# Performance work log

Hardware: AMD Instinct MI355X
Metric: run time of the kernel (lower is better)

Reference implementation:

```python
import jax, jax.numpy as jnp
import numpy as np

N = 10000      # nodes
E = 320000     # edges (avg degree 32)
D_IN = 128
D_H = 256
D_C = 32       # comm_dim
D_OUT = 64


def setup_inputs() -> dict:
    key = jax.random.key(0)
    ks = jax.random.split(key, 14)
    p = lambda k, shape: jax.random.normal(k, shape, jnp.float32) * 0.02
    return {
        "x": jax.random.normal(ks[0], (N, D_IN), jnp.float32),
        "edge_index": jax.random.randint(ks[1], (2, E), 0, N),
        "W_in": p(ks[2], (D_IN, D_H)), "b_in": jnp.zeros((D_H,), jnp.float32),
        "Wq": p(ks[3], (D_H, D_C)),   "bq": jnp.zeros((D_C,), jnp.float32),
        "Wk": p(ks[4], (D_H, D_C)),   "bk": jnp.zeros((D_C,), jnp.float32),
        "Wv": p(ks[5], (D_H, D_H)),   "bv": jnp.zeros((D_H,), jnp.float32),
        "W1": p(ks[6], (2 * D_H, D_H)), "b1": jnp.zeros((D_H,), jnp.float32),
        "W2": p(ks[7], (D_H, D_OUT)),  "b2": jnp.zeros((D_OUT,), jnp.float32),
    }


def reference(x, edge_index, W_in, b_in, Wq, bq, Wk, bk, Wv, bv, W1, b1, W2, b2):
    n = x.shape[0]
    h = x @ W_in + b_in                       # [N, D_H]
    q = h @ Wq + bq                           # [N, D_C]
    k = h @ Wk + bk                           # [N, D_C]
    v = h @ Wv + bv                           # [N, D_H]
    scores = (q @ k.T) / np.sqrt(q.shape[-1]).astype(np.float32)  # [N, N]
    # torch: zeros -> scatter 1 at edges -> masked_fill(==0, -inf);
    # edge positions keep value 1.0 ADDED to scores (faithful quirk).
    mask = jnp.full((n, n), -jnp.inf, jnp.float32)
    mask = mask.at[edge_index[0], edge_index[1]].set(1.0)
    w = jax.nn.softmax(scores + mask, axis=-1)
    w = jnp.nan_to_num(w, nan=0.0)            # rows with no edges -> all zeros
    comm = w @ v                              # [N, D_H]
    combined = jnp.concatenate([h, comm], axis=-1)  # [N, 2*D_H]
    return jax.nn.relu(combined @ W1 + b1) @ W2 + b2  # [N, D_OUT]
```

## Files before the change

### kernel.cpp

```cpp
#include <hip/hip_runtime.h>
#include <stdint.h>
#include <stddef.h>

constexpr int N_NODES = 10000;
constexpr int N_EDGES = 320000;
constexpr int DIM_IN  = 128;
constexpr int DIM_H   = 256;
constexpr int DIM_C   = 32;
constexpr int DIM_OUT = 64;
constexpr int DIM_QKV = DIM_C + DIM_C + DIM_H;
constexpr int DIM_QK  = 2 * DIM_C;
constexpr int DIM_CAT = 2 * DIM_H;
constexpr float SCALE = 0.17677669529663687f;
constexpr int MAXD = 192;
constexpr float VSCALE = 64.0f;
constexpr int PAD = 40;
constexpr int HP  = 264;

#if __has_builtin(__builtin_amdgcn_cvt_pk_f32_fp8) && __has_builtin(__builtin_amdgcn_cvt_pk_fp8_f32)
#define V_FP8 1
#else
#define V_FP8 0
#endif

constexpr size_t alignw(size_t w) { return (w + 15) & ~size_t(15); }
constexpr size_t OFF_DEG   = 0;
constexpr size_t OFF_COL   = alignw(OFF_DEG + N_NODES);
constexpr size_t OFF_QK    = alignw(OFF_COL + (size_t)N_NODES * MAXD);
constexpr size_t OFF_BQKV  = alignw(OFF_QK + (size_t)N_NODES * DIM_QK);
constexpr size_t OFF_VT    = alignw(OFF_BQKV + DIM_QKV);
constexpr size_t OFF_CATBF = alignw(OFF_VT + (size_t)N_NODES * DIM_H / 2);
constexpr size_t OFF_WINT  = alignw(OFF_CATBF + (size_t)N_NODES * DIM_CAT / 2);
constexpr size_t OFF_WQKVT = alignw(OFF_WINT + (size_t)DIM_H * DIM_IN / 2);
constexpr size_t OFF_W1T   = alignw(OFF_WQKVT + (size_t)DIM_QKV * DIM_H / 2);
constexpr size_t OFF_W2T   = alignw(OFF_W1T + (size_t)DIM_H * DIM_CAT / 2);

typedef __attribute__((ext_vector_type(8))) short short8;
typedef __attribute__((ext_vector_type(4))) float floatx4;
typedef __attribute__((ext_vector_type(2))) float floatx2;

#define MFMA16 __builtin_amdgcn_mfma_f32_16x16x32_bf16

__device__ inline unsigned short f2bf(float f) {
    uint32_t u = __builtin_bit_cast(uint32_t, f);
    uint32_t r = (u + 0x7fffu + ((u >> 16) & 1u)) >> 16;
    return (unsigned short)r;
}
__device__ inline float bf2f_lo(uint32_t u) { return __builtin_bit_cast(float, u << 16); }
__device__ inline float bf2f_hi(uint32_t u) { return __builtin_bit_cast(float, u & 0xffff0000u); }

__global__ void prep(const int* __restrict__ ei,
                     const float* __restrict__ W_in,
                     const float* __restrict__ Wq, const float* __restrict__ Wk,
                     const float* __restrict__ Wv,
                     const float* __restrict__ bq, const float* __restrict__ bk,
                     const float* __restrict__ bv,
                     const float* __restrict__ W1, const float* __restrict__ W2,
                     int* __restrict__ deg, int* __restrict__ col,
                     unsigned short* __restrict__ WinT, unsigned short* __restrict__ WqkvT,
                     unsigned short* __restrict__ W1T, unsigned short* __restrict__ W2T,
                     float* __restrict__ bqkv)
{
    const int i0 = blockIdx.x * blockDim.x + threadIdx.x;
    const int stride = gridDim.x * blockDim.x;
    for (int e = i0; e < N_EDGES; e += stride) {
        int src = ei[e];
        int dst = ei[N_EDGES + e];
        int slot = atomicAdd(&deg[src], 1);
        if (slot < MAXD) col[src * MAXD + slot] = dst;
    }
    for (int idx = i0; idx < DIM_IN * DIM_H; idx += stride) {
        int k = idx >> 8, n = idx & 255;
        WinT[n * DIM_IN + k] = f2bf(W_in[idx]);
    }
    for (int idx = i0; idx < DIM_H * DIM_C; idx += stride) {
        int k = idx >> 5, n = idx & 31;
        WqkvT[n * DIM_H + k] = f2bf(Wq[idx]);
    }
    for (int idx = i0; idx < DIM_H * DIM_C; idx += stride) {
        int k = idx >> 5, n = idx & 31;
        WqkvT[(DIM_C + n) * DIM_H + k] = f2bf(Wk[idx]);
    }
    for (int idx = i0; idx < DIM_H * DIM_H; idx += stride) {
        int k = idx >> 8, n = idx & 255;
        WqkvT[(2 * DIM_C + n) * DIM_H + k] = f2bf(Wv[idx]);
    }
    for (int idx = i0; idx < DIM_CAT * DIM_H; idx += stride) {
        int k = idx >> 8, n = idx & 255;
        W1T[n * DIM_CAT + k] = f2bf(W1[idx]);
    }
    for (int idx = i0; idx < DIM_H * DIM_OUT; idx += stride) {
        int k = idx >> 6, n = idx & 63;
        W2T[n * DIM_H + k] = f2bf(W2[idx]);
    }
    for (int idx = i0; idx < DIM_QKV; idx += stride)
        bqkv[idx] = (idx < DIM_C) ? bq[idx]
                  : (idx < 2 * DIM_C) ? bk[idx - DIM_C] : bv[idx - 2 * DIM_C];
}

__global__ __launch_bounds__(256)
void gemm12(const float* __restrict__ x,
            const unsigned short* __restrict__ WinT, const float* __restrict__ b_in,
            const unsigned short* __restrict__ WqkvT, const float* __restrict__ bqkv,
            unsigned short* __restrict__ cat_bf, float* __restrict__ qk,
            unsigned short* __restrict__ v_tab)
{
    __shared__ short hS[32 * HP];
    __shared__ short As[32 * PAD];
    __shared__ short Bs[320 * PAD];
    const int tid   = threadIdx.x;
    const int wave  = tid >> 6;
    const int lane  = tid & 63;
    const int quad  = lane >> 4;
    const int col16 = lane & 15;
    const int sr    = tid >> 2;
    const int sc    = (tid & 3) * 8;
    const int ar    = tid >> 3;
    const int ac    = (tid & 7) * 4;
    const int row0  = blockIdx.x * 32;

    floatx4 acc[2][4] = {};
    for (int k0 = 0; k0 < DIM_IN; k0 += 32) {
        {
            int gr = row0 + ar;
            float4 a = {};
            if (gr < N_NODES) a = *(const float4*)(x + (size_t)gr * DIM_IN + k0 + ac);
            uint2 o;
            o.x = (uint32_t)f2bf(a.x) | ((uint32_t)f2bf(a.y) << 16);
            o.y = (uint32_t)f2bf(a.z) | ((uint32_t)f2bf(a.w) << 16);
            *(uint2*)(As + ar * PAD + ac) = o;
        }
        #pragma unroll
        for (int p = 0; p < 4; ++p) {
            int r = sr + p * 64;
            *(short8*)(Bs + r * PAD + sc) = *(const short8*)(WinT + (size_t)r * DIM_IN + k0 + sc);
        }
        __syncthreads();
        short8 af[2], bfr[4];
        #pragma unroll
        for (int m = 0; m < 2; ++m)
            af[m] = *(const short8*)(As + (m * 16 + col16) * PAD + quad * 8);
        #pragma unroll
        for (int n = 0; n < 4; ++n)
            bfr[n] = *(const short8*)(Bs + (wave * 64 + n * 16 + col16) * PAD + quad * 8);
        #pragma unroll
        for (int m = 0; m < 2; ++m)
            #pragma unroll
            for (int n = 0; n < 4; ++n)
                acc[m][n] = MFMA16(af[m], bfr[n], acc[m][n], 0, 0, 0);
        __syncthreads();
    }
    #pragma unroll
    for (int m = 0; m < 2; ++m)
        #pragma unroll
        for (int n = 0; n < 4; ++n) {
            int gc = wave * 64 + n * 16 + col16;
            float bia = b_in[gc];
            #pragma unroll
            for (int r = 0; r < 4; ++r) {
                int lr = m * 16 + quad * 4 + r;
                unsigned short hv = f2bf(acc[m][n][r] + bia);
                hS[lr * HP + gc] = (short)hv;
                if (row0 + lr < N_NODES) cat_bf[(size_t)(row0 + lr) * DIM_CAT + gc] = hv;
            }
        }
    __syncthreads();

    floatx4 acc2[2][5] = {};
    for (int k0 = 0; k0 < DIM_H; k0 += 32) {
        #pragma unroll
        for (int p = 0; p < 5; ++p) {
            int r = sr + p * 64;
            *(short8*)(Bs + r * PAD + sc) = *(const short8*)(WqkvT + (size_t)r * DIM_H + k0 + sc);
        }
        __syncthreads();
        short8 af[2], bfr[5];
        #pragma unroll
        for (int m = 0; m < 2; ++m)
            af[m] = *(const short8*)(hS + (m * 16 + col16) * HP + k0 + quad * 8);
        #pragma unroll
        for (int n = 0; n < 5; ++n)
            bfr[n] = *(const short8*)(Bs + (wave * 80 + n * 16 + col16) * PAD + quad * 8);
        #pragma unroll
        for (int m = 0; m < 2; ++m)
            #pragma unroll
            for (int n = 0; n < 5; ++n)
                acc2[m][n] = MFMA16(af[m], bfr[n], acc2[m][n], 0, 0, 0);
        __syncthreads();
    }
    #pragma unroll
    for (int m = 0; m < 2; ++m)
        #pragma unroll
        for (int n = 0; n < 5; ++n) {
            int gc = wave * 80 + n * 16 + col16;
            float bia = bqkv[gc];
            #pragma unroll
            for (int r = 0; r < 4; ++r) {
                int gr = row0 + m * 16 + quad * 4 + r;
                if (gr >= N_NODES) continue;
                float v = acc2[m][n][r] + bia;
                if (gc < DIM_QK) {
                    qk[(size_t)gr * DIM_QK + gc] = v;
                } else {
#if V_FP8
                    int pk = __builtin_amdgcn_cvt_pk_fp8_f32(v * VSCALE, 0.f, 0, false);
                    ((unsigned char*)v_tab)[(size_t)gr * DIM_H + (gc - DIM_QK)] =
                        (unsigned char)(pk & 0xff);
#else
                    v_tab[(size_t)gr * DIM_H + (gc - DIM_QK)] = f2bf(v);
#endif
                }
            }
        }
}

__global__ __launch_bounds__(256)
void attn_row(const float* __restrict__ qk, const unsigned short* __restrict__ v_tab,
              const int* __restrict__ deg, const int* __restrict__ col,
              unsigned short* __restrict__ cat_bf) {
    __shared__ int   dstS[4][MAXD];
    __shared__ float wS[4][MAXD];
    __shared__ float qS[4][DIM_C];
    const int wave = threadIdx.x >> 6;
    const int lane = threadIdx.x & 63;
    const int row = blockIdx.x * 4 + wave;
    int d = deg[row];
    if (d > MAXD) d = MAXD;
    const int* crow = col + (size_t)row * MAXD;

    for (int p = lane; p < d; p += 64) dstS[wave][p] = crow[p];
    if (lane < DIM_C) qS[wave][lane] = qk[(size_t)row * DIM_QK + lane];
    __syncthreads();

    float mysum = 0.f;
    if (d <= 64) {
        int mydst = (lane < d) ? dstS[wave][lane] : -1;
        bool dup = false;
        for (int k2 = 0; k2 < d - 1; ++k2) {
            int other = __shfl(mydst, k2, 64);
            dup = dup || (k2 < lane && other == mydst);
        }
        float w = 0.f;
        if (lane < d && !dup) {
            const float4* kp = (const float4*)(qk + (size_t)mydst * DIM_QK + DIM_C);
            float s = 0.f;
            #pragma unroll
            for (int i = 0; i < DIM_C / 4; ++i) {
                float4 b = kp[i];
                s += qS[wave][4 * i + 0] * b.x + qS[wave][4 * i + 1] * b.y
                   + qS[wave][4 * i + 2] * b.z + qS[wave][4 * i + 3] * b.w;
            }
            w = expf(s * SCALE);
        }
        wS[wave][lane] = w;
        mysum = w;
    } else {
        for (int p = lane; p < d; p += 64) {
            int mydst = dstS[wave][p];
            bool dup = false;
            for (int j = 0; j < p; ++j) dup = dup || (dstS[wave][j] == mydst);
            float w = 0.f;
            if (!dup) {
                const float4* kp = (const float4*)(qk + (size_t)mydst * DIM_QK + DIM_C);
                float s = 0.f;
                #pragma unroll
                for (int i = 0; i < DIM_C / 4; ++i) {
                    float4 b = kp[i];
                    s += qS[wave][4 * i + 0] * b.x + qS[wave][4 * i + 1] * b.y
                       + qS[wave][4 * i + 2] * b.z + qS[wave][4 * i + 3] * b.w;
                }
                w = expf(s * SCALE);
            }
            wS[wave][p] = w;
            mysum += w;
        }
    }
    #pragma unroll
    for (int off = 32; off; off >>= 1) mysum += __shfl_down(mysum, off, 64);
    float total = __shfl(mysum, 0, 64);
#if V_FP8
    float inv = (d > 0 && total > 0.f) ? 1.0f / (total * VSCALE) : 0.f;
#else
    float inv = (d > 0 && total > 0.f) ? 1.0f / total : 0.f;
#endif
    __syncthreads();

    float4 acc = make_float4(0.f, 0.f, 0.f, 0.f);
#if V_FP8
    const uint32_t* vb = (const uint32_t*)v_tab;
#else
    const uint2* vb = (const uint2*)v_tab;
#endif
    for (int p0 = 0; p0 < d; p0 += 16) {
        int j[16]; float w[16];
        #pragma unroll
        for (int t = 0; t < 16; ++t) {
            int idx = p0 + t;
            bool in = idx < d;
            j[t] = in ? dstS[wave][idx] : 0;
            w[t] = in ? wS[wave][idx] : 0.f;
        }
#if V_FP8
        uint32_t r[16];
        #pragma unroll
        for (int t = 0; t < 16; ++t) r[t] = vb[(size_t)j[t] * 64 + lane];
        #pragma unroll
        for (int t = 0; t < 16; ++t) {
            floatx2 lo = __builtin_amdgcn_cvt_pk_f32_fp8(r[t], false);
            floatx2 hi = __builtin_amdgcn_cvt_pk_f32_fp8(r[t], true);
            acc.x += w[t] * lo.x; acc.y += w[t] * lo.y;
            acc.z += w[t] * hi.x; acc.w += w[t] * hi.y;
        }
#else
        uint2 r[16];
        #pragma unroll
        for (int t = 0; t < 16; ++t) r[t] = vb[(size_t)j[t] * 64 + lane];
        #pragma unroll
        for (int t = 0; t < 16; ++t) {
            acc.x += w[t] * bf2f_lo(r[t].x);
            acc.y += w[t] * bf2f_hi(r[t].x);
            acc.z += w[t] * bf2f_lo(r[t].y);
            acc.w += w[t] * bf2f_hi(r[t].y);
        }
#endif
    }
    acc.x *= inv; acc.y *= inv; acc.z *= inv; acc.w *= inv;
    uint2 o;
    o.x = (uint32_t)f2bf(acc.x) | ((uint32_t)f2bf(acc.y) << 16);
    o.y = (uint32_t)f2bf(acc.z) | ((uint32_t)f2bf(acc.w) << 16);
    *(uint2*)(cat_bf + (size_t)row * DIM_CAT + DIM_H + lane * 4) = o;
}

__global__ __launch_bounds__(256)
void gemm_w1w2(const unsigned short* __restrict__ cat, const unsigned short* __restrict__ W1T,
               const float* __restrict__ b1, const unsigned short* __restrict__ W2T,
               const float* __restrict__ b2, float* __restrict__ out, int M)
{
    constexpr int TP = 260;
    __shared__ short As[32 * PAD];
    __shared__ short BsTs[256 * PAD];
    short* Bs = BsTs;
    short* Ts = BsTs;
    const int tid   = threadIdx.x;
    const int wave  = tid >> 6;
    const int lane  = tid & 63;
    const int quad  = lane >> 4;
    const int col16 = lane & 15;
    const int row0  = blockIdx.x * 32;

    const int sr = tid >> 2;
    const int sc = (tid & 3) * 8;

    floatx4 acc[2][4] = {};
    for (int k0 = 0; k0 < DIM_CAT; k0 += 32) {
        if (sr < 32) {
            int gr = row0 + sr;
            short8 v = {};
            if (gr < M) v = *(const short8*)(cat + (size_t)gr * DIM_CAT + k0 + sc);
            *(short8*)(As + sr * PAD + sc) = v;
        }
        #pragma unroll
        for (int p = 0; p < 4; ++p) {
            int r = sr + p * 64;
            *(short8*)(Bs + r * PAD + sc) = *(const short8*)(W1T + (size_t)r * DIM_CAT + k0 + sc);
        }
        __syncthreads();
        short8 af[2], bfr[4];
        #pragma unroll
        for (int m = 0; m < 2; ++m)
            af[m] = *(const short8*)(As + (m * 16 + col16) * PAD + quad * 8);
        #pragma unroll
        for (int n = 0; n < 4; ++n)
            bfr[n] = *(const short8*)(Bs + (wave * 64 + n * 16 + col16) * PAD + quad * 8);
        #pragma unroll
        for (int m = 0; m < 2; ++m)
            #pragma unroll
            for (int n = 0; n < 4; ++n)
                acc[m][n] = MFMA16(af[m], bfr[n], acc[m][n], 0, 0, 0);
        __syncthreads();
    }

    #pragma unroll
    for (int m = 0; m < 2; ++m)
        #pragma unroll
        for (int n = 0; n < 4; ++n) {
            int gc = wave * 64 + n * 16 + col16;
            float bia = b1[gc];
            #pragma unroll
            for (int r = 0; r < 4; ++r) {
                int lr = m * 16 + quad * 4 + r;
                Ts[lr * TP + gc] = (short)f2bf(fmaxf(acc[m][n][r] + bia, 0.f));
            }
        }
    __syncthreads();

    floatx4 acc2[2] = {};
    for (int k0 = 0; k0 < DIM_H; k0 += 32) {
        short8 b = *(const short8*)(W2T + (size_t)(wave * 16 + col16) * DIM_H + k0 + quad * 8);
        #pragma unroll
        for (int m = 0; m < 2; ++m) {
            short8 a = *(const short8*)(Ts + (m * 16 + col16) * TP + k0 + quad * 8);
            acc2[m] = MFMA16(a, b, acc2[m], 0, 0, 0);
        }
    }
    #pragma unroll
    for (int m = 0; m < 2; ++m) {
        int gc = wave * 16 + col16;
        float bia = b2[gc];
        #pragma unroll
        for (int r = 0; r < 4; ++r) {
            int gr = row0 + m * 16 + quad * 4 + r;
            if (gr < M) out[(size_t)gr * DIM_OUT + gc] = acc2[m][r] + bia;
        }
    }
}

extern "C" void kernel_launch(void* const* d_in, const int* in_sizes, int n_in,
                              void* d_out, int out_size, void* d_ws, size_t ws_size,
                              hipStream_t stream) {
    (void)in_sizes; (void)n_in; (void)out_size; (void)ws_size;
    const float* x    = (const float*)d_in[0];
    const int*   ei   = (const int*)d_in[1];
    const float* W_in = (const float*)d_in[2];
    const float* b_in = (const float*)d_in[3];
    const float* Wq   = (const float*)d_in[4];
    const float* bq   = (const float*)d_in[5];
    const float* Wk   = (const float*)d_in[6];
    const float* bk   = (const float*)d_in[7];
    const float* Wv   = (const float*)d_in[8];
    const float* bv   = (const float*)d_in[9];
    const float* W1   = (const float*)d_in[10];
    const float* b1   = (const float*)d_in[11];
    const float* W2   = (const float*)d_in[12];
    const float* b2   = (const float*)d_in[13];
    float* out = (float*)d_out;

    uint32_t* ws      = (uint32_t*)d_ws;
    int*      deg     = (int*)(ws + OFF_DEG);
    int*      col     = (int*)(ws + OFF_COL);
    float*    qk      = (float*)(ws + OFF_QK);
    float*    bqkv    = (float*)(ws + OFF_BQKV);
    unsigned short* v_tab  = (unsigned short*)(ws + OFF_VT);
    unsigned short* cat_bf = (unsigned short*)(ws + OFF_CATBF);
    unsigned short* WinT   = (unsigned short*)(ws + OFF_WINT);
    unsigned short* WqkvT  = (unsigned short*)(ws + OFF_WQKVT);
    unsigned short* W1T    = (unsigned short*)(ws + OFF_W1T);
    unsigned short* W2T    = (unsigned short*)(ws + OFF_W2T);

    hipMemsetAsync(deg, 0, N_NODES * sizeof(int), stream);
    prep<<<640, 256, 0, stream>>>(ei, W_in, Wq, Wk, Wv, bq, bk, bv, W1, W2,
                                  deg, col, WinT, WqkvT, W1T, W2T, bqkv);
    gemm12<<<(N_NODES + 31) / 32, 256, 0, stream>>>(
        x, WinT, b_in, WqkvT, bqkv, cat_bf, qk, v_tab);
    attn_row<<<N_NODES / 4, 256, 0, stream>>>(qk, v_tab, deg, col, cat_bf);
    gemm_w1w2<<<(N_NODES + 31) / 32, 256, 0, stream>>>(
        cat_bf, W1T, b1, W2T, b2, out, N_NODES);
}
```

Measured before the change: 168.8 us.

## Fold edge bucketing and W1/W2 conversion into gemm12, double GEMM K-step

Removes the memset and moves edge bucketing (atomic degree counting and column scatter) and the W1/W2 bf16 transposes out of the prep kernel into the gemm12 kernel, so prep only zeroes degrees and converts W_in/Wqkv. The bias concatenation buffer is dropped in favour of per-column selection. All GEMM loops now use a 64-wide K tile with two MFMAs per fragment, halving the number of barriers. The intent is fewer launches and less serialized prep work. In exchange, gemm12 uses more shared memory and registers, which may reduce occupancy, and its prologue is now dominated by atomics.

```diff
diff --git a/kernel.cpp b/kernel.cpp
--- a/kernel.cpp
+++ b/kernel.cpp
@@ -14,8 +14,9 @@
 constexpr float SCALE = 0.17677669529663687f;
 constexpr int MAXD = 192;
 constexpr float VSCALE = 64.0f;
-constexpr int PAD = 40;
-constexpr int HP  = 264;
+constexpr int PAD  = 40;
+constexpr int PAD2 = 72;
+constexpr int HP   = 264;
 
 #if __has_builtin(__builtin_amdgcn_cvt_pk_f32_fp8) && __has_builtin(__builtin_amdgcn_cvt_pk_fp8_f32)
 #define V_FP8 1
@@ -27,8 +28,7 @@
 constexpr size_t OFF_DEG   = 0;
 constexpr size_t OFF_COL   = alignw(OFF_DEG + N_NODES);
 constexpr size_t OFF_QK    = alignw(OFF_COL + (size_t)N_NODES * MAXD);
-constexpr size_t OFF_BQKV  = alignw(OFF_QK + (size_t)N_NODES * DIM_QK);
-constexpr size_t OFF_VT    = alignw(OFF_BQKV + DIM_QKV);
+constexpr size_t OFF_VT    = alignw(OFF_QK + (size_t)N_NODES * DIM_QK);
 constexpr size_t OFF_CATBF = alignw(OFF_VT + (size_t)N_NODES * DIM_H / 2);
 constexpr size_t OFF_WINT  = alignw(OFF_CATBF + (size_t)N_NODES * DIM_CAT / 2);
 constexpr size_t OFF_WQKVT = alignw(OFF_WINT + (size_t)DIM_H * DIM_IN / 2);
@@ -49,26 +49,15 @@
 __device__ inline float bf2f_lo(uint32_t u) { return __builtin_bit_cast(float, u << 16); }
 __device__ inline float bf2f_hi(uint32_t u) { return __builtin_bit_cast(float, u & 0xffff0000u); }
 
-__global__ void prep(const int* __restrict__ ei,
-                     const float* __restrict__ W_in,
-                     const float* __restrict__ Wq, const float* __restrict__ Wk,
-                     const float* __restrict__ Wv,
-                     const float* __restrict__ bq, const float* __restrict__ bk,
-                     const float* __restrict__ bv,
-                     const float* __restrict__ W1, const float* __restrict__ W2,
-                     int* __restrict__ deg, int* __restrict__ col,
-                     unsigned short* __restrict__ WinT, unsigned short* __restrict__ WqkvT,
-                     unsigned short* __restrict__ W1T, unsigned short* __restrict__ W2T,
-                     float* __restrict__ bqkv)
+__global__ void prep_w(const float* __restrict__ W_in,
+                       const float* __restrict__ Wq, const float* __restrict__ Wk,
+                       const float* __restrict__ Wv,
+                       int* __restrict__ deg,
+                       unsigned short* __restrict__ WinT, unsigned short* __restrict__ WqkvT)
 {
     const int i0 = blockIdx.x * blockDim.x + threadIdx.x;
     const int stride = gridDim.x * blockDim.x;
-    for (int e = i0; e < N_EDGES; e += stride) {
-        int src = ei[e];
-        int dst = ei[N_EDGES + e];
-        int slot = atomicAdd(&deg[src], 1);
-        if (slot < MAXD) col[src * MAXD + slot] = dst;
-    }
+    for (int i = i0; i < N_NODES; i += stride) deg[i] = 0;
     for (int idx = i0; idx < DIM_IN * DIM_H; idx += stride) {
         int k = idx >> 8, n = idx & 255;
         WinT[n * DIM_IN + k] = f2bf(W_in[idx]);
@@ -85,69 +74,95 @@
         int k = idx >> 8, n = idx & 255;
         WqkvT[(2 * DIM_C + n) * DIM_H + k] = f2bf(Wv[idx]);
     }
-    for (int idx = i0; idx < DIM_CAT * DIM_H; idx += stride) {
-        int k = idx >> 8, n = idx & 255;
-        W1T[n * DIM_CAT + k] = f2bf(W1[idx]);
-    }
-    for (int idx = i0; idx < DIM_H * DIM_OUT; idx += stride) {
-        int k = idx >> 6, n = idx & 63;
-        W2T[n * DIM_H + k] = f2bf(W2[idx]);
-    }
-    for (int idx = i0; idx < DIM_QKV; idx += stride)
-        bqkv[idx] = (idx < DIM_C) ? bq[idx]
-                  : (idx < 2 * DIM_C) ? bk[idx - DIM_C] : bv[idx - 2 * DIM_C];
 }
 
 __global__ __launch_bounds__(256)
-void gemm12(const float* __restrict__ x,
+void gemm12(const float* __restrict__ x, const int* __restrict__ ei,
             const unsigned short* __restrict__ WinT, const float* __restrict__ b_in,
-            const unsigned short* __restrict__ WqkvT, const float* __restrict__ bqkv,
+            const unsigned short* __restrict__ WqkvT,
+            const float* __restrict__ bq, const float* __restrict__ bk,
+            const float* __restrict__ bv,
+            const float* __restrict__ W1, const float* __restrict__ W2,
+            int* __restrict__ deg, int* __restrict__ col,
             unsigned short* __restrict__ cat_bf, float* __restrict__ qk,
-            unsigned short* __restrict__ v_tab)
+            unsigned short* __restrict__ v_tab,
+            unsigned short* __restrict__ W1T, unsigned short* __restrict__ W2T)
 {
-    __shared__ short hS[32 * HP];
-    __shared__ short As[32 * PAD];
-    __shared__ short Bs[320 * PAD];
+    __shared__ alignas(16) char SMEM[62976];
+    short* hS  = (short*)SMEM;
+    short* As1 = (short*)(SMEM + 16896);
+    short* Bs1 = (short*)(SMEM + 21504);
+    short* Bs2 = (short*)(SMEM + 16896);
     const int tid   = threadIdx.x;
+    const int bid   = blockIdx.x;
     const int wave  = tid >> 6;
     const int lane  = tid & 63;
     const int quad  = lane >> 4;
     const int col16 = lane & 15;
-    const int sr    = tid >> 2;
-    const int sc    = (tid & 3) * 8;
-    const int ar    = tid >> 3;
-    const int ac    = (tid & 7) * 4;
-    const int row0  = blockIdx.x * 32;
+    const int sr    = tid >> 3;
+    const int sc    = (tid & 7) * 8;
+    const int row0  = bid * 32;
+
+    {
+        const int stride = gridDim.x * 256;
+        const int i0 = bid * 256 + tid;
+        int s4[4], d4[4]; bool ok[4];
+        #pragma unroll
+        for (int t = 0; t < 4; ++t) {
+            int e = i0 + t * stride;
+            ok[t] = e < N_EDGES;
+            s4[t] = ok[t] ? ei[e] : 0;
+            d4[t] = ok[t] ? ei[N_EDGES + e] : 0;
+        }
+        #pragma unroll
+        for (int t = 0; t < 4; ++t)
+            if (ok[t]) {
+                int slot = atomicAdd(&deg[s4[t]], 1);
+                if (slot < MAXD) col[s4[t] * MAXD + slot] = d4[t];
+            }
+    }
 
     floatx4 acc[2][4] = {};
-    for (int k0 = 0; k0 < DIM_IN; k0 += 32) {
+    for (int k0 = 0; k0 < DIM_IN; k0 += 64) {
         {
-            int gr = row0 + ar;
-            float4 a = {};
-            if (gr < N_NODES) a = *(const float4*)(x + (size_t)gr * DIM_IN + k0 + ac);
-            uint2 o;
+            int gr = row0 + sr;
+            float4 a = {}, b = {};
+            if (gr < N_NODES) {
+                const float4* xp = (const float4*)(x + (size_t)gr * DIM_IN + k0 + sc);
+                a = xp[0]; b = xp[1];
+            }
+            uint4 o;
             o.x = (uint32_t)f2bf(a.x) | ((uint32_t)f2bf(a.y) << 16);
             o.y = (uint32_t)f2bf(a.z) | ((uint32_t)f2bf(a.w) << 16);
-            *(uint2*)(As + ar * PAD + ac) = o;
-        }
-        #pragma unroll
-        for (int p = 0; p < 4; ++p) {
-            int r = sr + p * 64;
-            *(short8*)(Bs + r * PAD + sc) = *(const short8*)(WinT + (size_t)r * DIM_IN + k0 + sc);
-        }
-        __syncthreads();
-        short8 af[2], bfr[4];
-        #pragma unroll
-        for (int m = 0; m < 2; ++m)
-            af[m] = *(const short8*)(As + (m * 16 + col16) * PAD + quad * 8);
+            o.z = (uint32_t)f2bf(b.x) | ((uint32_t)f2bf(b.y) << 16);
+            o.w = (uint32_t)f2bf(b.z) | ((uint32_t)f2bf(b.w) << 16);
+            *(uint4*)(As1 + sr * PAD2 + sc) = o;
+        }
+        #pragma unroll
+        for (int p = 0; p < 8; ++p) {
+            int r = sr + p * 32;
+            *(short8*)(Bs1 + r * PAD2 + sc) =
+                *(const short8*)(WinT + (size_t)r * DIM_IN + k0 + sc);
+        }
+        __syncthreads();
+        short8 af[2][2], bfr[4][2];
+        #pragma unroll
+        for (int m = 0; m < 2; ++m)
+            #pragma unroll
+            for (int kh = 0; kh < 2; ++kh)
+                af[m][kh] = *(const short8*)(As1 + (m * 16 + col16) * PAD2 + kh * 32 + quad * 8);
         #pragma unroll
         for (int n = 0; n < 4; ++n)
-            bfr[n] = *(const short8*)(Bs + (wave * 64 + n * 16 + col16) * PAD + quad * 8);
+            #pragma unroll
+            for (int kh = 0; kh < 2; ++kh)
+                bfr[n][kh] = *(const short8*)(Bs1 + (wave * 64 + n * 16 + col16) * PAD2 + kh * 32 + quad * 8);
         #pragma unroll
         for (int m = 0; m < 2; ++m)
             #pragma unroll
             for (int n = 0; n < 4; ++n)
-                acc[m][n] = MFMA16(af[m], bfr[n], acc[m][n], 0, 0, 0);
+                #pragma unroll
+                for (int kh = 0; kh < 2; ++kh)
+                    acc[m][n] = MFMA16(af[m][kh], bfr[n][kh], acc[m][n], 0, 0, 0);
         __syncthreads();
     }
     #pragma unroll
@@ -167,25 +182,32 @@
     __syncthreads();
 
     floatx4 acc2[2][5] = {};
-    for (int k0 = 0; k0 < DIM_H; k0 += 32) {
-        #pragma unroll
-        for (int p = 0; p < 5; ++p) {
-            int r = sr + p * 64;
-            *(short8*)(Bs + r * PAD + sc) = *(const short8*)(WqkvT + (size_t)r * DIM_H + k0 + sc);
-        }
-        __syncthreads();
-        short8 af[2], bfr[5];
-        #pragma unroll
-        for (int m = 0; m < 2; ++m)
-            af[m] = *(const short8*)(hS + (m * 16 + col16) * HP + k0 + quad * 8);
+    for (int k0 = 0; k0 < DIM_H; k0 += 64) {
+        #pragma unroll
+        for (int p = 0; p < 10; ++p) {
+            int r = sr + p * 32;
+            *(short8*)(Bs2 + r * PAD2 + sc) =
+                *(const short8*)(WqkvT + (size_t)r * DIM_H + k0 + sc);
+        }
+        __syncthreads();
+        short8 af[2][2], bfr[5][2];
+        #pragma unroll
+        for (int m = 0; m < 2; ++m)
+            #pragma unroll
+            for (int kh = 0; kh < 2; ++kh)
+                af[m][kh] = *(const short8*)(hS + (m * 16 + col16) * HP + k0 + kh * 32 + quad * 8);
         #pragma unroll
         for (int n = 0; n < 5; ++n)
-            bfr[n] = *(const short8*)(Bs + (wave * 80 + n * 16 + col16) * PAD + quad * 8);
+            #pragma unroll
+            for (int kh = 0; kh < 2; ++kh)
+                bfr[n][kh] = *(const short8*)(Bs2 + (wave * 80 + n * 16 + col16) * PAD2 + kh * 32 + quad * 8);
         #pragma unroll
         for (int m = 0; m < 2; ++m)
             #pragma unroll
             for (int n = 0; n < 5; ++n)
-                acc2[m][n] = MFMA16(af[m], bfr[n], acc2[m][n], 0, 0, 0);
+                #pragma unroll
+                for (int kh = 0; kh < 2; ++kh)
+                    acc2[m][n] = MFMA16(af[m][kh], bfr[n][kh], acc2[m][n], 0, 0, 0);
         __syncthreads();
     }
     #pragma unroll
@@ -193,7 +215,7 @@
         #pragma unroll
         for (int n = 0; n < 5; ++n) {
             int gc = wave * 80 + n * 16 + col16;
-            float bia = bqkv[gc];
+            float bia = (gc < DIM_C) ? bq[gc] : (gc < DIM_QK) ? bk[gc - DIM_C] : bv[gc - DIM_QK];
             #pragma unroll
             for (int r = 0; r < 4; ++r) {
                 int gr = row0 + m * 16 + quad * 4 + r;
@@ -212,6 +234,19 @@
                 }
             }
         }
+
+    {
+        const int stride = gridDim.x * 256;
+        const int i0 = bid * 256 + tid;
+        for (int idx = i0; idx < DIM_CAT * DIM_H; idx += stride) {
+            int k = idx >> 8, n = idx & 255;
+            W1T[n * DIM_CAT + k] = f2bf(W1[idx]);
+        }
+        for (int idx = i0; idx < DIM_H * DIM_OUT; idx += stride) {
+            int k = idx >> 6, n = idx & 63;
+            W2T[n * DIM_H + k] = f2bf(W2[idx]);
+        }
+    }
 }
 
 __global__ __launch_bounds__(256)
@@ -337,8 +372,8 @@
                const float* __restrict__ b2, float* __restrict__ out, int M)
 {
     constexpr int TP = 260;
-    __shared__ short As[32 * PAD];
-    __shared__ short BsTs[256 * PAD];
+    __shared__ short As[32 * PAD2];
+    __shared__ short BsTs[256 * PAD2];
     short* Bs = BsTs;
     short* Ts = BsTs;
     const int tid   = threadIdx.x;
@@ -348,35 +383,41 @@
     const int col16 = lane & 15;
     const int row0  = blockIdx.x * 32;
 
-    const int sr = tid >> 2;
-    const int sc = (tid & 3) * 8;
+    const int sr = tid >> 3;
+    const int sc = (tid & 7) * 8;
 
     floatx4 acc[2][4] = {};
-    for (int k0 = 0; k0 < DIM_CAT; k0 += 32) {
-        if (sr < 32) {
+    for (int k0 = 0; k0 < DIM_CAT; k0 += 64) {
+        {
             int gr = row0 + sr;
             short8 v = {};
             if (gr < M) v = *(const short8*)(cat + (size_t)gr * DIM_CAT + k0 + sc);
-            *(short8*)(As + sr * PAD + sc) = v;
-        }
-        #pragma unroll
-        for (int p = 0; p < 4; ++p) {
-            int r = sr + p * 64;
-            *(short8*)(Bs + r * PAD + sc) = *(const short8*)(W1T + (size_t)r * DIM_CAT + k0 + sc);
-        }
-        __syncthreads();
-        short8 af[2], bfr[4];
-        #pragma unroll
-        for (int m = 0; m < 2; ++m)
-            af[m] = *(const short8*)(As + (m * 16 + col16) * PAD + quad * 8);
+            *(short8*)(As + sr * PAD2 + sc) = v;
+        }
+        #pragma unroll
+        for (int p = 0; p < 8; ++p) {
+            int r = sr + p * 32;
+            *(short8*)(Bs + r * PAD2 + sc) = *(const short8*)(W1T + (size_t)r * DIM_CAT + k0 + sc);
+        }
+        __syncthreads();
+        short8 af[2][2], bfr[4][2];
+        #pragma unroll
+        for (int m = 0; m < 2; ++m)
+            #pragma unroll
+            for (int kh = 0; kh < 2; ++kh)
+                af[m][kh] = *(const short8*)(As + (m * 16 + col16) * PAD2 + kh * 32 + quad * 8);
         #pragma unroll
         for (int n = 0; n < 4; ++n)
-            bfr[n] = *(const short8*)(Bs + (wave * 64 + n * 16 + col16) * PAD + quad * 8);
+            #pragma unroll
+            for (int kh = 0; kh < 2; ++kh)
+                bfr[n][kh] = *(const short8*)(Bs + (wave * 64 + n * 16 + col16) * PAD2 + kh * 32 + quad * 8);
         #pragma unroll
         for (int m = 0; m < 2; ++m)
             #pragma unroll
             for (int n = 0; n < 4; ++n)
-                acc[m][n] = MFMA16(af[m], bfr[n], acc[m][n], 0, 0, 0);
+                #pragma unroll
+                for (int kh = 0; kh < 2; ++kh)
+                    acc[m][n] = MFMA16(af[m][kh], bfr[n][kh], acc[m][n], 0, 0, 0);
         __syncthreads();
     }
 
@@ -439,7 +480,6 @@
     int*      deg     = (int*)(ws + OFF_DEG);
     int*      col     = (int*)(ws + OFF_COL);
     float*    qk      = (float*)(ws + OFF_QK);
-    float*    bqkv    = (float*)(ws + OFF_BQKV);
     unsigned short* v_tab  = (unsigned short*)(ws + OFF_VT);
     unsigned short* cat_bf = (unsigned short*)(ws + OFF_CATBF);
     unsigned short* WinT   = (unsigned short*)(ws + OFF_WINT);
@@ -447,11 +487,10 @@
     unsigned short* W1T    = (unsigned short*)(ws + OFF_W1T);
     unsigned short* W2T    = (unsigned short*)(ws + OFF_W2T);
 
-    hipMemsetAsync(deg, 0, N_NODES * sizeof(int), stream);
-    prep<<<640, 256, 0, stream>>>(ei, W_in, Wq, Wk, Wv, bq, bk, bv, W1, W2,
-                                  deg, col, WinT, WqkvT, W1T, W2T, bqkv);
+    prep_w<<<256, 256, 0, stream>>>(W_in, Wq, Wk, Wv, deg, WinT, WqkvT);
     gemm12<<<(N_NODES + 31) / 32, 256, 0, stream>>>(
-        x, WinT, b_in, WqkvT, bqkv, cat_bf, qk, v_tab);
+        x, ei, WinT, b_in, WqkvT, bq, bk, bv, W1, W2,
+        deg, col, cat_bf, qk, v_tab, W1T, W2T);
     attn_row<<<N_NODES / 4, 256, 0, stream>>>(qk, v_tab, deg, col, cat_bf);
     gemm_w1w2<<<(N_NODES + 31) / 32, 256, 0, stream>>>(
         cat_bf, W1T, b1, W2T, b2, out, N_NODES);
```

Result: no change. 166.7 us (-1.3%).
